# Performance work log

Hardware: AMD Instinct MI355X
Metric: run time of the kernel (lower is better)

## Reference

```python
import jax, jax.numpy as jnp
import numpy as np

D_K, D_MODEL, NUM_HEADS = 64, 1024, 16


def _xavier(key, shape):
    # xavier_uniform over last two dims (fan_in=shape[-2], fan_out=shape[-1])
    fan_in, fan_out = shape[-2], shape[-1]
    limit = float(np.sqrt(6.0 / (fan_in + fan_out)))
    return jax.random.uniform(key, shape, jnp.float32, -limit, limit)


def setup_inputs() -> dict:
    key = jax.random.key(0)
    kx, kq, kk, kv, ko = jax.random.split(key, 5)
    x = jax.random.normal(kx, (2, 2048, D_MODEL), dtype=jnp.float32)
    w_q = _xavier(kq, (NUM_HEADS, D_MODEL, D_K))
    w_k = _xavier(kk, (NUM_HEADS, D_MODEL, D_K))
    w_v = _xavier(kv, (NUM_HEADS, D_MODEL, D_K))
    w_o = _xavier(ko, (NUM_HEADS * D_K, D_MODEL))
    return {"x": x, "w_q": w_q, "w_k": w_k, "w_v": w_v, "w_o": w_o}


def reference(x, w_q, w_k, w_v, w_o):
    scale = 1.0 / jnp.sqrt(jnp.asarray(D_K, dtype=jnp.float32))
    q = jnp.einsum('bsd,hdk->bhsk', x, w_q)
    k = jnp.einsum('bsd,hdk->bhsk', x, w_k)
    v = jnp.einsum('bsd,hdk->bhsk', x, w_v)
    scores = jnp.einsum('bhqk,bhmk->bhqm', q, k) * scale  # [B,H,S,S]
    weights = jax.nn.softmax(scores, axis=-1)
    z = jnp.einsum('bhqm,bhmk->bhqk', weights, v)
    b, h, s, dk = z.shape
    z = jnp.transpose(z, (0, 2, 1, 3)).reshape(b, s, h * dk)
    z = jnp.einsum('bse,ed->bsd', z, w_o)
    return x + z  # dropout_prob=0.0 (eval): identity
```

## Files before the change

kernel.cpp:

```cpp
#include <hip/hip_runtime.h>
#include <hip/hip_bf16.h>
#include <stdint.h>

typedef float    f32x4  __attribute__((ext_vector_type(4)));
typedef __bf16   bf16x8 __attribute__((ext_vector_type(8)));
typedef uint16_t u16;

#define NHEADS 16
#define DKV    64
#define DMODEL 1024
#define BATCH  2
#define SEQ    2048
#define ROWS   4096

#define EXP2F(x) __builtin_amdgcn_exp2f(x)

__device__ __forceinline__ u16 f2bf(float f) {
  union { float f; uint32_t u; } v; v.f = f;
  uint32_t r = v.u + 0x7fffu + ((v.u >> 16) & 1u);
  return (u16)(r >> 16);
}

__device__ __forceinline__ void gload16(const void* g, void* l) {
  __builtin_amdgcn_global_load_lds(
      (const __attribute__((address_space(1))) uint32_t*)g,
      (__attribute__((address_space(3))) uint32_t*)l, 16, 0, 0);
}

__device__ __forceinline__ f32x4 mfma16(bf16x8 a, bf16x8 b, f32x4 c) {
  return __builtin_amdgcn_mfma_f32_16x16x32_bf16(a, b, c, 0, 0, 0);
}

__global__ void cast_x_kernel(const float* __restrict__ x, u16* __restrict__ xb) {
  int i = blockIdx.x * 256 + threadIdx.x;
  const float4* p = (const float4*)(x + (size_t)i * 8);
  float4 a = p[0], b = p[1];
  u16* o = xb + (size_t)i * 8;
  u16 tmp[8] = { f2bf(a.x), f2bf(a.y), f2bf(a.z), f2bf(a.w),
                 f2bf(b.x), f2bf(b.y), f2bf(b.z), f2bf(b.w) };
  *(uint4*)o = *(uint4*)tmp;
}

__global__ void wtrans_kernel(const float* __restrict__ wq, const float* __restrict__ wk,
                              const float* __restrict__ wv, const float* __restrict__ wo,
                              u16* __restrict__ wt, u16* __restrict__ wot) {
  __shared__ float t[64][65];
  int blk = blockIdx.x, tid = threadIdx.x;
  const float* src; u16* dst; int sld, dld;
  if (blk < 768) {
    int p = blk >> 8, rem = blk & 255;
    int h = rem >> 4, dt = rem & 15;
    const float* w = (p == 0) ? wq : (p == 1) ? wk : wv;
    src = w + ((size_t)h * 1024 + dt * 64) * 64;   sld = 64;
    dst = wt + ((size_t)(p * 1024 + h * 64)) * 1024 + dt * 64; dld = 1024;
  } else {
    int t2 = blk - 768, rt = t2 >> 4, ct = t2 & 15;
    src = wo + (size_t)(rt * 64) * 1024 + ct * 64;  sld = 1024;
    dst = wot + (size_t)(ct * 64) * 1024 + rt * 64; dld = 1024;
  }
#pragma unroll
  for (int i = 0; i < 16; i++) {
    int e = tid + i * 256, r = e >> 6, c = e & 63;
    t[r][c] = src[(size_t)r * sld + c];
  }
  __syncthreads();
#pragma unroll
  for (int i = 0; i < 16; i++) {
    int e = tid + i * 256, r = e >> 6, c = e & 63;
    dst[(size_t)r * dld + c] = f2bf(t[c][r]);
  }
}

template<int EPI>
__global__ __launch_bounds__(256) void gemm_bt(
    const u16* __restrict__ A, const u16* __restrict__ Bt, int K, int ntn,
    u16* __restrict__ qout, u16* __restrict__ kout, u16* __restrict__ vout,
    const float* __restrict__ xres, float* __restrict__ fout) {
  __shared__ __align__(16) u16 As[128 * 32];
  __shared__ __align__(16) u16 Bs[128 * 32];
  int tid = threadIdx.x, l = tid & 63, w = tid >> 6;
  int bid = blockIdx.x;
  int m0 = (bid / ntn) * 128, n0 = (bid % ntn) * 128;
  int wm = (w >> 1) * 64, wn = (w & 1) * 64;
  int cg = l >> 4, cl = l & 15;
  int lrow = l >> 2, lcol = l & 3;

  f32x4 acc[4][4];
#pragma unroll
  for (int i = 0; i < 4; i++)
#pragma unroll
    for (int j = 0; j < 4; j++) acc[i][j] = (f32x4){0.f, 0.f, 0.f, 0.f};

  for (int k0 = 0; k0 < K; k0 += 32) {
    __syncthreads();
    const u16* ga = A  + (size_t)(m0 + w * 16 + lrow) * K + k0 + lcol * 8;
    const u16* gb = Bt + (size_t)(n0 + w * 16 + lrow) * K + k0 + lcol * 8;
    gload16(ga,            &As[(w * 16) * 32]);
    gload16(ga + 64 * (size_t)K, &As[(w * 16 + 64) * 32]);
    gload16(gb,            &Bs[(w * 16) * 32]);
    gload16(gb + 64 * (size_t)K, &Bs[(w * 16 + 64) * 32]);
    __syncthreads();

    bf16x8 af[4], bfr[4];
#pragma unroll
    for (int mi = 0; mi < 4; mi++)
      af[mi] = *(const bf16x8*)&As[(wm + mi * 16 + cl) * 32 + cg * 8];
#pragma unroll
    for (int ni = 0; ni < 4; ni++)
      bfr[ni] = *(const bf16x8*)&Bs[(wn + ni * 16 + cl) * 32 + cg * 8];
#pragma unroll
    for (int mi = 0; mi < 4; mi++)
#pragma unroll
      for (int ni = 0; ni < 4; ni++)
        acc[mi][ni] = mfma16(af[mi], bfr[ni], acc[mi][ni]);
  }

#pragma unroll
  for (int mi = 0; mi < 4; mi++)
#pragma unroll
    for (int ni = 0; ni < 4; ni++) {
      int nbase = n0 + wn + ni * 16 + cl;
#pragma unroll
      for (int r = 0; r < 4; r++) {
        int m = m0 + wm + mi * 16 + cg * 4 + r;
        float v = acc[mi][ni][r];
        if (EPI == 0) {
          int p = nbase >> 10, hh = (nbase >> 6) & 15, dk = nbase & 63;
          int b = m >> 11, s = m & 2047;
          size_t o = ((size_t)((b * 16 + hh)) * 2048 + s) * 64 + dk;
          u16* dst = (p == 0) ? qout : (p == 1) ? kout : vout;
          dst[o] = f2bf((p == 0) ? v * 0.18033688f : v);
        } else {
          size_t o = (size_t)m * 1024 + nbase;
          fout[o] = v + xres[o];
        }
      }
    }
}

__global__ void vtrans_kernel(const u16* __restrict__ v, u16* __restrict__ vt) {
  __shared__ u16 t[64][68];
  int blk = blockIdx.x, tid = threadIdx.x;
  int bh = blk >> 5, st = blk & 31;
  const u16* src = v + ((size_t)bh * 2048 + st * 64) * 64;
  u16* dst = vt + ((size_t)bh * 64) * 2048 + st * 64;
#pragma unroll
  for (int i = 0; i < 16; i++) {
    int e = tid + i * 256, r = e >> 6, c = e & 63;
    t[r][c] = src[(size_t)r * 64 + c];
  }
  __syncthreads();
#pragma unroll
  for (int i = 0; i < 16; i++) {
    int e = tid + i * 256, r = e >> 6, c = e & 63;
    dst[(size_t)r * 2048 + c] = t[c][r];
  }
}

__global__ __launch_bounds__(512) void attn_kernel(
    const u16* __restrict__ q, const u16* __restrict__ k,
    const u16* __restrict__ vt, u16* __restrict__ z) {
  __shared__ __align__(16) u16 Ks[2][64 * 64];
  __shared__ __align__(16) u16 Vs[2][64 * 64];
  __shared__ __align__(16) u16 Ps[8][16 * 64];
  int tid = threadIdx.x, l = tid & 63, w = tid >> 6;
  int blk = blockIdx.x;
  int xcd = blk & 7, slot = blk >> 3;
  int bh = xcd + 8 * (slot >> 4), qt = slot & 15;
  int b = bh >> 4, h = bh & 15;
  int q0 = qt * 128 + w * 16;
  int cg = l >> 4, cl = l & 15;
  int swz = (cl & 7) << 4;

  const u16* qb = q  + ((size_t)bh * 2048 + q0) * 64;
  const u16* kb = k  + (size_t)bh * 2048 * 64;
  const u16* vb = vt + (size_t)bh * 64 * 2048;

  int srow = w * 8 + (l >> 3);
  int scb  = (l & 7) ^ (l >> 3);

  bf16x8 bq0 = *(const bf16x8*)&qb[(size_t)cl * 64 + cg * 8];
  bf16x8 bq1 = *(const bf16x8*)&qb[(size_t)cl * 64 + 32 + cg * 8];

  f32x4 oacc[4];
#pragma unroll
  for (int i = 0; i < 4; i++) oacc[i] = (f32x4){0.f, 0.f, 0.f, 0.f};
  float mrun = -3.0e38f, lrun = 0.f;

  gload16(kb + (size_t)srow * 64 + scb * 8,   &Ks[0][(w * 8) * 64]);
  gload16(vb + (size_t)srow * 2048 + scb * 8, &Vs[0][(w * 8) * 64]);
  __syncthreads();

  for (int t = 0; t < 32; t++) {
    int cur = t & 1, nxt = cur ^ 1;
    if (t + 1 < 32) {
      gload16(kb + ((size_t)(t + 1) * 64 + srow) * 64 + scb * 8,  &Ks[nxt][(w * 8) * 64]);
      gload16(vb + (size_t)srow * 2048 + (t + 1) * 64 + scb * 8,  &Vs[nxt][(w * 8) * 64]);
    }

    f32x4 sc[4];
#pragma unroll
    for (int g = 0; g < 4; g++) {
      const char* kp = (const char*)&Ks[cur][(g * 16 + cl) * 64];
      bf16x8 a0 = *(const bf16x8*)(kp + ((cg * 16)      ^ swz));
      bf16x8 a1 = *(const bf16x8*)(kp + ((cg * 16 + 64) ^ swz));
      f32x4 t2 = (f32x4){0.f, 0.f, 0.f, 0.f};
      t2 = mfma16(a0, bq0, t2);
      t2 = mfma16(a1, bq1, t2);
      sc[g] = t2;
    }

    float m01 = fmaxf(fmaxf(sc[0][0], sc[0][1]), fmaxf(sc[0][2], sc[0][3]));
    float m23 = fmaxf(fmaxf(sc[1][0], sc[1][1]), fmaxf(sc[1][2], sc[1][3]));
    float m45 = fmaxf(fmaxf(sc[2][0], sc[2][1]), fmaxf(sc[2][2], sc[2][3]));
    float m67 = fmaxf(fmaxf(sc[3][0], sc[3][1]), fmaxf(sc[3][2], sc[3][3]));
    float mx = fmaxf(fmaxf(m01, m23), fmaxf(m45, m67));
    mx = fmaxf(mx, __shfl_xor(mx, 16));
    mx = fmaxf(mx, __shfl_xor(mx, 32));
    float mnew = fmaxf(mrun, mx);
    float fac = EXP2F(mrun - mnew);
    mrun = mnew;
    float rs = 0.f;
#pragma unroll
    for (int g = 0; g < 4; g++)
#pragma unroll
      for (int r = 0; r < 4; r++) {
        float p = EXP2F(sc[g][r] - mnew);
        sc[g][r] = p;
        rs += p;
      }
    rs += __shfl_xor(rs, 16);
    rs += __shfl_xor(rs, 32);
    lrun = lrun * fac + rs;
#pragma unroll
    for (int nd = 0; nd < 4; nd++)
#pragma unroll
      for (int r = 0; r < 4; r++) oacc[nd][r] *= fac;

    char* pw = (char*)&Ps[w][cl * 64];
#pragma unroll
    for (int g = 0; g < 4; g++) {
      uint32_t lo = (uint32_t)f2bf(sc[g][0]) | ((uint32_t)f2bf(sc[g][1]) << 16);
      uint32_t hi = (uint32_t)f2bf(sc[g][2]) | ((uint32_t)f2bf(sc[g][3]) << 16);
      *(uint2*)(pw + ((g * 32 + cg * 8) ^ swz)) = make_uint2(lo, hi);
    }
    bf16x8 pb0 = *(const bf16x8*)(pw + ((cg * 16)      ^ swz));
    bf16x8 pb1 = *(const bf16x8*)(pw + ((cg * 16 + 64) ^ swz));

#pragma unroll
    for (int nd = 0; nd < 4; nd++) {
      const char* vp = (const char*)&Vs[cur][(nd * 16 + cl) * 64];
      bf16x8 v0 = *(const bf16x8*)(vp + ((cg * 16)      ^ swz));
      bf16x8 v1 = *(const bf16x8*)(vp + ((cg * 16 + 64) ^ swz));
      oacc[nd] = mfma16(v0, pb0, oacc[nd]);
      oacc[nd] = mfma16(v1, pb1, oacc[nd]);
    }

    __syncthreads();
  }

  float inv = 1.0f / lrun;
  u16* zb = z + ((size_t)(b * 2048) + q0) * 1024 + h * 64;
#pragma unroll
  for (int nd = 0; nd < 4; nd++) {
    uint32_t lo = (uint32_t)f2bf(oacc[nd][0] * inv) | ((uint32_t)f2bf(oacc[nd][1] * inv) << 16);
    uint32_t hi = (uint32_t)f2bf(oacc[nd][2] * inv) | ((uint32_t)f2bf(oacc[nd][3] * inv) << 16);
    *(uint2*)&zb[(size_t)cl * 1024 + nd * 16 + cg * 4] = make_uint2(lo, hi);
  }
}

extern "C" void kernel_launch(void* const* d_in, const int* in_sizes, int n_in,
                              void* d_out, int out_size, void* d_ws, size_t ws_size,
                              hipStream_t stream) {
  const float* x  = (const float*)d_in[0];
  const float* wq = (const float*)d_in[1];
  const float* wk = (const float*)d_in[2];
  const float* wv = (const float*)d_in[3];
  const float* wo = (const float*)d_in[4];
  float* out = (float*)d_out;

  uint8_t* ws = (uint8_t*)d_ws;
  u16* xb  = (u16*)(ws);
  u16* wt  = (u16*)(ws + (8ull  << 20));
  u16* wot = (u16*)(ws + (14ull << 20));
  u16* qb  = (u16*)(ws + (16ull << 20));
  u16* kb  = (u16*)(ws + (24ull << 20));
  u16* vb  = (u16*)(ws + (32ull << 20));
  u16* vt  = (u16*)(ws + (40ull << 20));
  u16* zb  = (u16*)(ws + (48ull << 20));
  if (ws_size < (56ull << 20)) return;

  cast_x_kernel<<<2048, 256, 0, stream>>>(x, xb);
  wtrans_kernel<<<1024, 256, 0, stream>>>(wq, wk, wv, wo, wt, wot);
  gemm_bt<0><<<768, 256, 0, stream>>>(xb, wt, 1024, 24, qb, kb, vb, nullptr, nullptr);
  vtrans_kernel<<<1024, 256, 0, stream>>>(vb, vt);
  attn_kernel<<<512, 512, 0, stream>>>(qb, kb, vt, zb);
  gemm_bt<1><<<256, 256, 0, stream>>>(zb, wot, 1024, 8, nullptr, nullptr, nullptr, x, out);
}
```

Before: 212.1 us.

## Fuse prep kernels, write V transposed from GEMM, lazy softmax rescale, XCD remap

Merges the x cast and weight transpose into one prep kernel and has the QKV GEMM epilogue write V directly in transposed layout, which removes the separate V transpose kernel and its extra memory pass. The attention kernel now rescales only when the running max grows by more than a threshold (lazy rescaling), raises wave priority around the MFMA blocks, and packs bf16 pairs with hardware conversion instead of manual rounding. GEMM blocks are remapped so consecutive tiles land on the same XCD for L2 locality. The transposed V store from the GEMM is strided and may coalesce poorly.

```diff
diff --git a/kernel.cpp b/kernel.cpp
--- a/kernel.cpp
+++ b/kernel.cpp
@@ -4,6 +4,7 @@
 
 typedef float    f32x4  __attribute__((ext_vector_type(4)));
 typedef __bf16   bf16x8 __attribute__((ext_vector_type(8)));
+typedef __bf16   bf16x2 __attribute__((ext_vector_type(2)));
 typedef uint16_t u16;
 
 #define NHEADS 16
@@ -16,9 +17,13 @@
 #define EXP2F(x) __builtin_amdgcn_exp2f(x)
 
 __device__ __forceinline__ u16 f2bf(float f) {
-  union { float f; uint32_t u; } v; v.f = f;
-  uint32_t r = v.u + 0x7fffu + ((v.u >> 16) & 1u);
-  return (u16)(r >> 16);
+  __bf16 h = (__bf16)f;
+  union { __bf16 h; u16 u; } c; c.h = h; return c.u;
+}
+__device__ __forceinline__ uint32_t pk2(float a, float b) {
+  union { bf16x2 v; uint32_t u; } c;
+  c.v = (bf16x2){(__bf16)a, (__bf16)b};
+  return c.u;
 }
 
 __device__ __forceinline__ void gload16(const void* g, void* l) {
@@ -31,30 +36,32 @@
   return __builtin_amdgcn_mfma_f32_16x16x32_bf16(a, b, c, 0, 0, 0);
 }
 
-__global__ void cast_x_kernel(const float* __restrict__ x, u16* __restrict__ xb) {
-  int i = blockIdx.x * 256 + threadIdx.x;
-  const float4* p = (const float4*)(x + (size_t)i * 8);
-  float4 a = p[0], b = p[1];
-  u16* o = xb + (size_t)i * 8;
-  u16 tmp[8] = { f2bf(a.x), f2bf(a.y), f2bf(a.z), f2bf(a.w),
-                 f2bf(b.x), f2bf(b.y), f2bf(b.z), f2bf(b.w) };
-  *(uint4*)o = *(uint4*)tmp;
-}
-
-__global__ void wtrans_kernel(const float* __restrict__ wq, const float* __restrict__ wk,
-                              const float* __restrict__ wv, const float* __restrict__ wo,
-                              u16* __restrict__ wt, u16* __restrict__ wot) {
+__global__ void prep_kernel(const float* __restrict__ x, u16* __restrict__ xb,
+                            const float* __restrict__ wq, const float* __restrict__ wk,
+                            const float* __restrict__ wv, const float* __restrict__ wo,
+                            u16* __restrict__ wt, u16* __restrict__ wot) {
+  int blk = blockIdx.x, tid = threadIdx.x;
+  if (blk < 2048) {
+    int i = blk * 256 + tid;
+    const float4* p = (const float4*)(x + (size_t)i * 8);
+    float4 a = p[0], b = p[1];
+    uint32_t o0 = pk2(a.x, a.y), o1 = pk2(a.z, a.w);
+    uint32_t o2 = pk2(b.x, b.y), o3 = pk2(b.z, b.w);
+    uint4 pk = make_uint4(o0, o1, o2, o3);
+    *(uint4*)(xb + (size_t)i * 8) = pk;
+    return;
+  }
   __shared__ float t[64][65];
-  int blk = blockIdx.x, tid = threadIdx.x;
+  int wblk = blk - 2048;
   const float* src; u16* dst; int sld, dld;
-  if (blk < 768) {
-    int p = blk >> 8, rem = blk & 255;
+  if (wblk < 768) {
+    int p = wblk >> 8, rem = wblk & 255;
     int h = rem >> 4, dt = rem & 15;
     const float* w = (p == 0) ? wq : (p == 1) ? wk : wv;
     src = w + ((size_t)h * 1024 + dt * 64) * 64;   sld = 64;
     dst = wt + ((size_t)(p * 1024 + h * 64)) * 1024 + dt * 64; dld = 1024;
   } else {
-    int t2 = blk - 768, rt = t2 >> 4, ct = t2 & 15;
+    int t2 = wblk - 768, rt = t2 >> 4, ct = t2 & 15;
     src = wo + (size_t)(rt * 64) * 1024 + ct * 64;  sld = 1024;
     dst = wot + (size_t)(ct * 64) * 1024 + rt * 64; dld = 1024;
   }
@@ -79,7 +86,8 @@
   __shared__ __align__(16) u16 As[128 * 32];
   __shared__ __align__(16) u16 Bs[128 * 32];
   int tid = threadIdx.x, l = tid & 63, w = tid >> 6;
-  int bid = blockIdx.x;
+  int nwg = gridDim.x, cpx = nwg >> 3;
+  int bid = (blockIdx.x & 7) * cpx + (blockIdx.x >> 3);
   int m0 = (bid / ntn) * 128, n0 = (bid % ntn) * 128;
   int wm = (w >> 1) * 64, wn = (w & 1) * 64;
   int cg = l >> 4, cl = l & 15;
@@ -127,34 +135,20 @@
         if (EPI == 0) {
           int p = nbase >> 10, hh = (nbase >> 6) & 15, dk = nbase & 63;
           int b = m >> 11, s = m & 2047;
-          size_t o = ((size_t)((b * 16 + hh)) * 2048 + s) * 64 + dk;
-          u16* dst = (p == 0) ? qout : (p == 1) ? kout : vout;
-          dst[o] = f2bf((p == 0) ? v * 0.18033688f : v);
+          int bh = b * 16 + hh;
+          if (p == 2) {
+            vout[((size_t)bh * 64 + dk) * 2048 + s] = f2bf(v);
+          } else {
+            size_t o = ((size_t)bh * 2048 + s) * 64 + dk;
+            u16* dst = (p == 0) ? qout : kout;
+            dst[o] = f2bf((p == 0) ? v * 0.18033688f : v);
+          }
         } else {
           size_t o = (size_t)m * 1024 + nbase;
           fout[o] = v + xres[o];
         }
       }
     }
-}
-
-__global__ void vtrans_kernel(const u16* __restrict__ v, u16* __restrict__ vt) {
-  __shared__ u16 t[64][68];
-  int blk = blockIdx.x, tid = threadIdx.x;
-  int bh = blk >> 5, st = blk & 31;
-  const u16* src = v + ((size_t)bh * 2048 + st * 64) * 64;
-  u16* dst = vt + ((size_t)bh * 64) * 2048 + st * 64;
-#pragma unroll
-  for (int i = 0; i < 16; i++) {
-    int e = tid + i * 256, r = e >> 6, c = e & 63;
-    t[r][c] = src[(size_t)r * 64 + c];
-  }
-  __syncthreads();
-#pragma unroll
-  for (int i = 0; i < 16; i++) {
-    int e = tid + i * 256, r = e >> 6, c = e & 63;
-    dst[(size_t)r * 2048 + c] = t[c][r];
-  }
 }
 
 __global__ __launch_bounds__(512) void attn_kernel(
@@ -199,6 +193,7 @@
     }
 
     f32x4 sc[4];
+    __builtin_amdgcn_s_setprio(1);
 #pragma unroll
     for (int g = 0; g < 4; g++) {
       const char* kp = (const char*)&Ks[cur][(g * 16 + cl) * 64];
@@ -209,6 +204,7 @@
       t2 = mfma16(a1, bq1, t2);
       sc[g] = t2;
     }
+    __builtin_amdgcn_s_setprio(0);
 
     float m01 = fmaxf(fmaxf(sc[0][0], sc[0][1]), fmaxf(sc[0][2], sc[0][3]));
     float m23 = fmaxf(fmaxf(sc[1][0], sc[1][1]), fmaxf(sc[1][2], sc[1][3]));
@@ -217,36 +213,40 @@
     float mx = fmaxf(fmaxf(m01, m23), fmaxf(m45, m67));
     mx = fmaxf(mx, __shfl_xor(mx, 16));
     mx = fmaxf(mx, __shfl_xor(mx, 32));
-    float mnew = fmaxf(mrun, mx);
-    float fac = EXP2F(mrun - mnew);
-    mrun = mnew;
+    if (!__all(mx <= mrun + 8.0f)) {
+      float mnew = fmaxf(mrun, mx);
+      float fac = EXP2F(mrun - mnew);
+      mrun = mnew;
+      lrun *= fac;
+#pragma unroll
+      for (int nd = 0; nd < 4; nd++)
+#pragma unroll
+        for (int r = 0; r < 4; r++) oacc[nd][r] *= fac;
+    }
     float rs = 0.f;
 #pragma unroll
     for (int g = 0; g < 4; g++)
 #pragma unroll
       for (int r = 0; r < 4; r++) {
-        float p = EXP2F(sc[g][r] - mnew);
+        float p = EXP2F(sc[g][r] - mrun);
         sc[g][r] = p;
         rs += p;
       }
     rs += __shfl_xor(rs, 16);
     rs += __shfl_xor(rs, 32);
-    lrun = lrun * fac + rs;
-#pragma unroll
-    for (int nd = 0; nd < 4; nd++)
-#pragma unroll
-      for (int r = 0; r < 4; r++) oacc[nd][r] *= fac;
+    lrun += rs;
 
     char* pw = (char*)&Ps[w][cl * 64];
 #pragma unroll
     for (int g = 0; g < 4; g++) {
-      uint32_t lo = (uint32_t)f2bf(sc[g][0]) | ((uint32_t)f2bf(sc[g][1]) << 16);
-      uint32_t hi = (uint32_t)f2bf(sc[g][2]) | ((uint32_t)f2bf(sc[g][3]) << 16);
+      uint32_t lo = pk2(sc[g][0], sc[g][1]);
+      uint32_t hi = pk2(sc[g][2], sc[g][3]);
       *(uint2*)(pw + ((g * 32 + cg * 8) ^ swz)) = make_uint2(lo, hi);
     }
     bf16x8 pb0 = *(const bf16x8*)(pw + ((cg * 16)      ^ swz));
     bf16x8 pb1 = *(const bf16x8*)(pw + ((cg * 16 + 64) ^ swz));
 
+    __builtin_amdgcn_s_setprio(1);
 #pragma unroll
     for (int nd = 0; nd < 4; nd++) {
       const char* vp = (const char*)&Vs[cur][(nd * 16 + cl) * 64];
@@ -255,6 +255,7 @@
       oacc[nd] = mfma16(v0, pb0, oacc[nd]);
       oacc[nd] = mfma16(v1, pb1, oacc[nd]);
     }
+    __builtin_amdgcn_s_setprio(0);
 
     __syncthreads();
   }
@@ -263,8 +264,8 @@
   u16* zb = z + ((size_t)(b * 2048) + q0) * 1024 + h * 64;
 #pragma unroll
   for (int nd = 0; nd < 4; nd++) {
-    uint32_t lo = (uint32_t)f2bf(oacc[nd][0] * inv) | ((uint32_t)f2bf(oacc[nd][1] * inv) << 16);
-    uint32_t hi = (uint32_t)f2bf(oacc[nd][2] * inv) | ((uint32_t)f2bf(oacc[nd][3] * inv) << 16);
+    uint32_t lo = pk2(oacc[nd][0] * inv, oacc[nd][1] * inv);
+    uint32_t hi = pk2(oacc[nd][2] * inv, oacc[nd][3] * inv);
     *(uint2*)&zb[(size_t)cl * 1024 + nd * 16 + cg * 4] = make_uint2(lo, hi);
   }
 }
@@ -285,15 +286,12 @@
   u16* wot = (u16*)(ws + (14ull << 20));
   u16* qb  = (u16*)(ws + (16ull << 20));
   u16* kb  = (u16*)(ws + (24ull << 20));
-  u16* vb  = (u16*)(ws + (32ull << 20));
-  u16* vt  = (u16*)(ws + (40ull << 20));
-  u16* zb  = (u16*)(ws + (48ull << 20));
-  if (ws_size < (56ull << 20)) return;
-
-  cast_x_kernel<<<2048, 256, 0, stream>>>(x, xb);
-  wtrans_kernel<<<1024, 256, 0, stream>>>(wq, wk, wv, wo, wt, wot);
-  gemm_bt<0><<<768, 256, 0, stream>>>(xb, wt, 1024, 24, qb, kb, vb, nullptr, nullptr);
-  vtrans_kernel<<<1024, 256, 0, stream>>>(vb, vt);
+  u16* vt  = (u16*)(ws + (32ull << 20));
+  u16* zb  = (u16*)(ws + (40ull << 20));
+  if (ws_size < (48ull << 20)) return;
+
+  prep_kernel<<<3072, 256, 0, stream>>>(x, xb, wq, wk, wv, wo, wt, wot);
+  gemm_bt<0><<<768, 256, 0, stream>>>(xb, wt, 1024, 24, qb, kb, vt, nullptr, nullptr);
   attn_kernel<<<512, 512, 0, stream>>>(qb, kb, vt, zb);
   gemm_bt<1><<<256, 256, 0, stream>>>(zb, wot, 1024, 8, nullptr, nullptr, nullptr, x, out);
 }
```

Result: faster. 207.6 us (-2.1%).
